# Kernel tuning notes

Measured on AMD Instinct MI355X. Metric: run time of the kernel, lower is better.

The kernel has to match this reference:

```python
import jax, jax.numpy as jnp
import numpy as np

B, N, DH = 8, 2048, 512
EPS = 1e-5


def _layer_norm(x, g, b):
    m = x.mean(-1, keepdims=True)
    v = ((x - m) ** 2).mean(-1, keepdims=True)
    return (x - m) * jax.lax.rsqrt(v + EPS) * g + b


def setup_inputs() -> dict:
    key = jax.random.key(0)
    ks = jax.random.split(key, 20)
    s = 1.0 / np.sqrt(DH)
    sf = 1.0 / np.sqrt(2 * DH)
    return {
        "H": jax.random.normal(ks[0], (B, N, DH), jnp.float32),
        "adj": jax.random.uniform(ks[1], (B, N, N), jnp.float32),
        "hop_emb": jax.random.normal(ks[2], (N, DH), jnp.float32),
        "Wq": jax.random.normal(ks[3], (DH, DH), jnp.float32) * s,
        "bq": jnp.zeros((DH,), jnp.float32),
        "Wk": jax.random.normal(ks[4], (DH, DH), jnp.float32) * s,
        "bk": jnp.zeros((DH,), jnp.float32),
        "Wv": jax.random.normal(ks[5], (DH, DH), jnp.float32) * s,
        "bv": jnp.zeros((DH,), jnp.float32),
        "W1": jax.random.normal(ks[6], (DH, 2 * DH), jnp.float32) * s,
        "b1": jnp.zeros((2 * DH,), jnp.float32),
        "W2": jax.random.normal(ks[7], (2 * DH, DH), jnp.float32) * sf,
        "b2": jnp.zeros((DH,), jnp.float32),
        "g1": jnp.ones((DH,), jnp.float32),
        "be1": jnp.zeros((DH,), jnp.float32),
        "g2": jnp.ones((DH,), jnp.float32),
        "be2": jnp.zeros((DH,), jnp.float32),
    }


def reference(H, adj, hop_emb, Wq, bq, Wk, bk, Wv, bv, W1, b1, W2, b2, g1, be1, g2, be2):
    Q = H @ Wq + bq                                     # [B,N,DH]
    K = H @ Wk + bk
    V = H @ Wv + bv
    scores = jnp.einsum("bid,bjd->bij", Q, K) / np.sqrt(DH).astype(np.float32)
    # (adj[...,None] * hop_emb).mean(-1) == adj * hop_emb.mean(-1)[j]
    hop_effect = adj * hop_emb.mean(-1)[None, None, :]  # [B,N,N]
    attn = jax.nn.softmax(scores * hop_effect, axis=-1)
    attn_out = jnp.einsum("bij,bjd->bid", attn, V)
    x = _layer_norm(attn_out + H, g1, be1)
    ffn = jax.nn.relu(x @ W1 + b1) @ W2 + b2
    return _layer_norm(ffn + x, g2, be2)
```

## Files before the change

kernel.cpp:

```cpp
#include <hip/hip_runtime.h>

typedef unsigned short u16;
typedef __bf16 bf16x8 __attribute__((ext_vector_type(8)));
typedef float f32x4 __attribute__((ext_vector_type(4)));

#define SEQN 2048
#define DHID 512

static __device__ __forceinline__ float bf2f(u16 u) {
    union { unsigned int i; float f; } c; c.i = ((unsigned int)u) << 16; return c.f;
}
static __device__ __forceinline__ u16 f2bf(float f) {
    union { float f; unsigned int i; } c; c.f = f;
    unsigned int x = c.i;
    return (u16)((x + 0x7fffu + ((x >> 16) & 1u)) >> 16);
}

static __device__ __forceinline__ void gld_lds16(const u16* g, u16* l) {
    __builtin_amdgcn_global_load_lds(
        (__attribute__((address_space(1))) void*)(g),
        (__attribute__((address_space(3))) void*)(l), 16, 0, 0);
}

__global__ __launch_bounds__(256) void cvt_kernel(const float* __restrict__ src,
                                                  u16* __restrict__ dst, int n) {
    int i = (blockIdx.x * 256 + threadIdx.x) * 8;
    if (i >= n) return;
    float4 a = *(const float4*)(src + i);
    float4 b = *(const float4*)(src + i + 4);
    union { uint4 u; u16 s[8]; } o;
    o.s[0] = f2bf(a.x); o.s[1] = f2bf(a.y); o.s[2] = f2bf(a.z); o.s[3] = f2bf(a.w);
    o.s[4] = f2bf(b.x); o.s[5] = f2bf(b.y); o.s[6] = f2bf(b.z); o.s[7] = f2bf(b.w);
    *(uint4*)(dst + i) = o.u;
}

__global__ __launch_bounds__(256) void cvt_t_kernel(const float* __restrict__ src,
                                                    u16* __restrict__ dst, int K, int N) {
    int idx = blockIdx.x * 256 + threadIdx.x;
    if (idx >= K * N) return;
    int n = idx / K, k = idx - n * K;
    dst[idx] = f2bf(src[(size_t)k * N + n]);
}

__global__ void hmean_kernel(const float* __restrict__ hop, float* __restrict__ hm) {
    int j = blockIdx.x, t = threadIdx.x;
    const float* p = hop + (size_t)j * DHID + t * 8;
    float4 a = *(const float4*)p;
    float4 b = *(const float4*)(p + 4);
    float s = a.x + a.y + a.z + a.w + b.x + b.y + b.z + b.w;
#pragma unroll
    for (int m = 1; m < 64; m <<= 1) s += __shfl_xor(s, m);
    if (t == 0) hm[j] = s * (1.0f / (float)DHID);
}

enum { EPI_BIAS = 0, EPI_RELU = 1, EPI_SCORES = 2, EPI_PLAIN = 3, EPI_BIAS_T = 4 };

template <int EPI>
__global__ __launch_bounds__(256) void gemm_bt(
    const u16* __restrict__ A, const u16* __restrict__ Bt, u16* __restrict__ C,
    const float* __restrict__ bias, const float* __restrict__ adj,
    const float* __restrict__ hmean,
    int K, int lda, int ldb, int ldc,
    long sA, long sB, long sC, long sAdj, float scale)
{
    __shared__ u16 As[128 * 32];
    __shared__ u16 Bs[128 * 32];

    const int tid = threadIdx.x;
    const int bz = blockIdx.z;
    const u16* Ab = A + (size_t)bz * sA;
    const u16* Bb = Bt + (size_t)bz * sB;
    u16* Cb = C + (size_t)bz * sC;

    const int bm0 = blockIdx.y * 128, bn0 = blockIdx.x * 128;
    const int wid = tid >> 6, lane = tid & 63, quad = lane >> 4, l16 = lane & 15;
    const int wm = (wid >> 1) * 64, wn = (wid & 1) * 64;
    const int srow = lane >> 2;
    const int skof = (lane & 3) * 8;

    f32x4 acc[4][4];
#pragma unroll
    for (int i = 0; i < 4; ++i)
#pragma unroll
        for (int j = 0; j < 4; ++j) acc[i][j] = (f32x4){0.f, 0.f, 0.f, 0.f};

    for (int k0 = 0; k0 < K; k0 += 32) {
#pragma unroll
        for (int it = 0; it < 2; ++it) {
            int c = wid * 2 + it;
            gld_lds16(Ab + (size_t)(bm0 + c * 16 + srow) * lda + k0 + skof,
                      &As[c * 512]);
        }
#pragma unroll
        for (int it = 0; it < 2; ++it) {
            int c = wid * 2 + it;
            gld_lds16(Bb + (size_t)(bn0 + c * 16 + srow) * ldb + k0 + skof,
                      &Bs[c * 512]);
        }
        __syncthreads();

        bf16x8 af[4], bfr[4];
#pragma unroll
        for (int i = 0; i < 4; ++i)
            af[i] = *(const bf16x8*)&As[(wm + i * 16 + l16) * 32 + quad * 8];
#pragma unroll
        for (int j = 0; j < 4; ++j)
            bfr[j] = *(const bf16x8*)&Bs[(wn + j * 16 + l16) * 32 + quad * 8];
#pragma unroll
        for (int i = 0; i < 4; ++i)
#pragma unroll
            for (int j = 0; j < 4; ++j)
                acc[i][j] = __builtin_amdgcn_mfma_f32_16x16x32_bf16(af[i], bfr[j], acc[i][j], 0, 0, 0);
        __syncthreads();
    }

#pragma unroll
    for (int i = 0; i < 4; ++i) {
#pragma unroll
        for (int j = 0; j < 4; ++j) {
            const int gn = bn0 + wn + j * 16 + l16;
            const int gm0 = bm0 + wm + i * 16 + quad * 4;
            if constexpr (EPI == EPI_BIAS || EPI == EPI_RELU) {
                const float b = bias[gn];
#pragma unroll
                for (int r = 0; r < 4; ++r) {
                    float v = acc[i][j][r] + b;
                    if constexpr (EPI == EPI_RELU) v = fmaxf(v, 0.f);
                    Cb[(size_t)(gm0 + r) * ldc + gn] = f2bf(v);
                }
            } else if constexpr (EPI == EPI_SCORES) {
                const float* adjb = adj + (size_t)bz * sAdj;
                const float hmn = hmean[gn];
#pragma unroll
                for (int r = 0; r < 4; ++r) {
                    float v = acc[i][j][r] * scale * adjb[(size_t)(gm0 + r) * ldc + gn] * hmn;
                    Cb[(size_t)(gm0 + r) * ldc + gn] = f2bf(v);
                }
            } else if constexpr (EPI == EPI_BIAS_T) {
                const float b = bias[gn];
                const int bb = gm0 >> 11, n = gm0 & 2047;
                ushort4 o;
                o.x = f2bf(acc[i][j][0] + b);
                o.y = f2bf(acc[i][j][1] + b);
                o.z = f2bf(acc[i][j][2] + b);
                o.w = f2bf(acc[i][j][3] + b);
                *(ushort4*)&C[((size_t)bb * 512 + gn) * 2048 + n] = o;
            } else {
#pragma unroll
                for (int r = 0; r < 4; ++r)
                    Cb[(size_t)(gm0 + r) * ldc + gn] = f2bf(acc[i][j][r]);
            }
        }
    }
}

__global__ __launch_bounds__(256) void softmax_kernel(u16* __restrict__ S) {
    size_t row = blockIdx.x;
    u16* p = S + row * (size_t)SEQN;
    int t = threadIdx.x, wid = t >> 6, lane = t & 63;

    union { uint4 u; u16 s[8]; } d;
    d.u = *(const uint4*)(p + t * 8);
    float v[8];
    float mx = -1e30f;
#pragma unroll
    for (int i = 0; i < 8; ++i) { v[i] = bf2f(d.s[i]); mx = fmaxf(mx, v[i]); }
#pragma unroll
    for (int m = 1; m < 64; m <<= 1) mx = fmaxf(mx, __shfl_xor(mx, m));
    __shared__ float redm[4], reds[4];
    if (lane == 0) redm[wid] = mx;
    __syncthreads();
    mx = fmaxf(fmaxf(redm[0], redm[1]), fmaxf(redm[2], redm[3]));

    float s = 0.f;
#pragma unroll
    for (int i = 0; i < 8; ++i) { v[i] = __expf(v[i] - mx); s += v[i]; }
#pragma unroll
    for (int m = 1; m < 64; m <<= 1) s += __shfl_xor(s, m);
    if (lane == 0) reds[wid] = s;
    __syncthreads();
    s = reds[0] + reds[1] + reds[2] + reds[3];
    float inv = 1.f / s;
#pragma unroll
    for (int i = 0; i < 8; ++i) d.s[i] = f2bf(v[i] * inv);
    *(uint4*)(p + t * 8) = d.u;
}

template <bool B_F32, bool OUT_F32>
__global__ __launch_bounds__(256) void ln_kernel(
    const u16* __restrict__ a, const void* __restrict__ bp,
    const float* __restrict__ g, const float* __restrict__ be,
    void* __restrict__ out)
{
    size_t row = blockIdx.x;
    int t = threadIdx.x, wid = t >> 6, lane = t & 63;
    const u16* pa = a + row * (size_t)DHID;

    unsigned int va = *(const unsigned int*)(pa + t * 2);
    float b0, b1;
    if constexpr (B_F32) {
        float2 vb = *(const float2*)((const float*)bp + row * (size_t)DHID + t * 2);
        b0 = vb.x; b1 = vb.y;
    } else {
        unsigned int vb = *(const unsigned int*)((const u16*)bp + row * (size_t)DHID + t * 2);
        b0 = bf2f((u16)(vb & 0xffff)); b1 = bf2f((u16)(vb >> 16));
    }
    float x0 = bf2f((u16)(va & 0xffff)) + b0;
    float x1 = bf2f((u16)(va >> 16)) + b1;
    float s = x0 + x1, sq = x0 * x0 + x1 * x1;
#pragma unroll
    for (int m = 1; m < 64; m <<= 1) { s += __shfl_xor(s, m); sq += __shfl_xor(sq, m); }
    __shared__ float rs[4], rq[4];
    if (lane == 0) { rs[wid] = s; rq[wid] = sq; }
    __syncthreads();
    s = rs[0] + rs[1] + rs[2] + rs[3];
    sq = rq[0] + rq[1] + rq[2] + rq[3];
    float mean = s * (1.f / (float)DHID);
    float var = sq * (1.f / (float)DHID) - mean * mean;
    float rstd = rsqrtf(var + 1e-5f);

    float2 vg = *(const float2*)(g + t * 2);
    float2 vbe = *(const float2*)(be + t * 2);
    float y0 = (x0 - mean) * rstd * vg.x + vbe.x;
    float y1 = (x1 - mean) * rstd * vg.y + vbe.y;
    if constexpr (OUT_F32) {
        *(float2*)((float*)out + row * (size_t)DHID + t * 2) = make_float2(y0, y1);
    } else {
        unsigned int o = (unsigned int)f2bf(y0) | ((unsigned int)f2bf(y1) << 16);
        *(unsigned int*)((u16*)out + row * (size_t)DHID + t * 2) = o;
    }
}

extern "C" void kernel_launch(void* const* d_in, const int* in_sizes, int n_in,
                              void* d_out, int out_size, void* d_ws, size_t ws_size,
                              hipStream_t stream) {
    const float* H   = (const float*)d_in[0];
    const float* adj = (const float*)d_in[1];
    const float* hop = (const float*)d_in[2];
    const float* Wq  = (const float*)d_in[3];
    const float* bq  = (const float*)d_in[4];
    const float* Wk  = (const float*)d_in[5];
    const float* bk  = (const float*)d_in[6];
    const float* Wv  = (const float*)d_in[7];
    const float* bv  = (const float*)d_in[8];
    const float* W1  = (const float*)d_in[9];
    const float* b1  = (const float*)d_in[10];
    const float* W2  = (const float*)d_in[11];
    const float* b2  = (const float*)d_in[12];
    const float* g1  = (const float*)d_in[13];
    const float* be1 = (const float*)d_in[14];
    const float* g2  = (const float*)d_in[15];
    const float* be2 = (const float*)d_in[16];

    const size_t MiB = 1ull << 20;
    char* w = (char*)d_ws;
    float* hm  = (float*)w;
    u16* Hb   = (u16*)(w + 1 * MiB);
    u16* Wqt  = (u16*)(w + 17 * MiB);
    u16* Wkt  = (u16*)(w + 17 * MiB + 512 * 1024);
    u16* Wvt  = (u16*)(w + 18 * MiB);
    u16* W1t  = (u16*)(w + 18 * MiB + 512 * 1024);
    u16* W2t  = (u16*)(w + 19 * MiB + 512 * 1024);
    u16* Q    = (u16*)(w + 21 * MiB);
    u16* Kb   = (u16*)(w + 37 * MiB);
    u16* Vt   = (u16*)(w + 53 * MiB);
    u16* S    = (u16*)(w + 69 * MiB);
    u16* AO  = Q;
    u16* X   = Kb;
    u16* F2  = Vt;
    u16* HID = S;

    const int BN = 8, N = SEQN, D = DHID;
    const long nd = (long)N * D, nn = (long)N * N;
    const float scale = 0.044194173824159216f;

    const int groups = (ws_size >= 133 * MiB) ? 1 : 2;
    const int gb = BN / groups;

    cvt_kernel<<<(BN * N * D) / (8 * 256), 256, 0, stream>>>(H, Hb, BN * N * D);
    cvt_t_kernel<<<(D * D + 255) / 256, 256, 0, stream>>>(Wq, Wqt, D, D);
    cvt_t_kernel<<<(D * D + 255) / 256, 256, 0, stream>>>(Wk, Wkt, D, D);
    cvt_t_kernel<<<(D * D + 255) / 256, 256, 0, stream>>>(Wv, Wvt, D, D);
    cvt_t_kernel<<<(D * 2 * D + 255) / 256, 256, 0, stream>>>(W1, W1t, D, 2 * D);
    cvt_t_kernel<<<(2 * D * D + 255) / 256, 256, 0, stream>>>(W2, W2t, 2 * D, D);

    hmean_kernel<<<N, 64, 0, stream>>>(hop, hm);

    gemm_bt<EPI_BIAS><<<dim3(4, 128, 1), 256, 0, stream>>>(
        Hb, Wqt, Q, bq, nullptr, nullptr, D, D, D, D, 0, 0, 0, 0, 0.f);
    gemm_bt<EPI_BIAS><<<dim3(4, 128, 1), 256, 0, stream>>>(
        Hb, Wkt, Kb, bk, nullptr, nullptr, D, D, D, D, 0, 0, 0, 0, 0.f);
    gemm_bt<EPI_BIAS_T><<<dim3(4, 128, 1), 256, 0, stream>>>(
        Hb, Wvt, Vt, bv, nullptr, nullptr, D, D, D, D, 0, 0, 0, 0, 0.f);

    for (int g = 0; g < groups; ++g) {
        const u16* Qg = Q + (size_t)g * gb * nd;
        const u16* Kg = Kb + (size_t)g * gb * nd;
        const u16* Vg = Vt + (size_t)g * gb * nd;
        const float* adjg = adj + (size_t)g * gb * nn;
        u16* AOg = AO + (size_t)g * gb * nd;

        gemm_bt<EPI_SCORES><<<dim3(16, 16, gb), 256, 0, stream>>>(
            Qg, Kg, S, nullptr, adjg, hm, D, D, D, N, nd, nd, nn, nn, scale);

        softmax_kernel<<<gb * N, 256, 0, stream>>>(S);

        gemm_bt<EPI_PLAIN><<<dim3(4, 16, gb), 256, 0, stream>>>(
            S, Vg, AOg, nullptr, nullptr, nullptr, N, N, N, D, nn, nd, nd, 0, 0.f);
    }

    ln_kernel<true, false><<<BN * N, 256, 0, stream>>>(AO, H, g1, be1, X);

    gemm_bt<EPI_RELU><<<dim3(8, 128, 1), 256, 0, stream>>>(
        X, W1t, HID, b1, nullptr, nullptr, D, D, D, 2 * D, 0, 0, 0, 0, 0.f);

    gemm_bt<EPI_BIAS><<<dim3(4, 128, 1), 256, 0, stream>>>(
        HID, W2t, F2, b2, nullptr, nullptr, 2 * D, 2 * D, 2 * D, D, 0, 0, 0, 0, 0.f);

    ln_kernel<false, true><<<BN * N, 256, 0, stream>>>(F2, X, g2, be2, (float*)d_out);
}
```

Baseline: 589.6 us.

## Fuse scores, softmax and PV into a single flash-style attention kernel

Result: no change. 595.9 us (+1.1%).

```diff
diff --git a/kernel.cpp b/kernel.cpp
--- a/kernel.cpp
+++ b/kernel.cpp
@@ -53,15 +53,14 @@
     if (t == 0) hm[j] = s * (1.0f / (float)DHID);
 }
 
-enum { EPI_BIAS = 0, EPI_RELU = 1, EPI_SCORES = 2, EPI_PLAIN = 3, EPI_BIAS_T = 4 };
+enum { EPI_BIAS = 0, EPI_RELU = 1, EPI_PLAIN = 3, EPI_BIAS_T = 4 };
 
 template <int EPI>
 __global__ __launch_bounds__(256) void gemm_bt(
     const u16* __restrict__ A, const u16* __restrict__ Bt, u16* __restrict__ C,
-    const float* __restrict__ bias, const float* __restrict__ adj,
-    const float* __restrict__ hmean,
+    const float* __restrict__ bias,
     int K, int lda, int ldb, int ldc,
-    long sA, long sB, long sC, long sAdj, float scale)
+    long sA, long sB, long sC)
 {
     __shared__ u16 As[128 * 32];
     __shared__ u16 Bs[128 * 32];
@@ -126,14 +125,6 @@
                 for (int r = 0; r < 4; ++r) {
                     float v = acc[i][j][r] + b;
                     if constexpr (EPI == EPI_RELU) v = fmaxf(v, 0.f);
-                    Cb[(size_t)(gm0 + r) * ldc + gn] = f2bf(v);
-                }
-            } else if constexpr (EPI == EPI_SCORES) {
-                const float* adjb = adj + (size_t)bz * sAdj;
-                const float hmn = hmean[gn];
-#pragma unroll
-                for (int r = 0; r < 4; ++r) {
-                    float v = acc[i][j][r] * scale * adjb[(size_t)(gm0 + r) * ldc + gn] * hmn;
                     Cb[(size_t)(gm0 + r) * ldc + gn] = f2bf(v);
                 }
             } else if constexpr (EPI == EPI_BIAS_T) {
@@ -154,36 +145,118 @@
     }
 }
 
-__global__ __launch_bounds__(256) void softmax_kernel(u16* __restrict__ S) {
-    size_t row = blockIdx.x;
-    u16* p = S + row * (size_t)SEQN;
-    int t = threadIdx.x, wid = t >> 6, lane = t & 63;
-
-    union { uint4 u; u16 s[8]; } d;
-    d.u = *(const uint4*)(p + t * 8);
-    float v[8];
-    float mx = -1e30f;
-#pragma unroll
-    for (int i = 0; i < 8; ++i) { v[i] = bf2f(d.s[i]); mx = fmaxf(mx, v[i]); }
-#pragma unroll
-    for (int m = 1; m < 64; m <<= 1) mx = fmaxf(mx, __shfl_xor(mx, m));
-    __shared__ float redm[4], reds[4];
-    if (lane == 0) redm[wid] = mx;
-    __syncthreads();
-    mx = fmaxf(fmaxf(redm[0], redm[1]), fmaxf(redm[2], redm[3]));
-
-    float s = 0.f;
-#pragma unroll
-    for (int i = 0; i < 8; ++i) { v[i] = __expf(v[i] - mx); s += v[i]; }
-#pragma unroll
-    for (int m = 1; m < 64; m <<= 1) s += __shfl_xor(s, m);
-    if (lane == 0) reds[wid] = s;
-    __syncthreads();
-    s = reds[0] + reds[1] + reds[2] + reds[3];
-    float inv = 1.f / s;
-#pragma unroll
-    for (int i = 0; i < 8; ++i) d.s[i] = f2bf(v[i] * inv);
-    *(uint4*)(p + t * 8) = d.u;
+__global__ __launch_bounds__(256, 1) void attn_kernel(
+    const u16* __restrict__ Q, const u16* __restrict__ K, const u16* __restrict__ Vt,
+    const float* __restrict__ adj, const float* __restrict__ hm,
+    u16* __restrict__ AO)
+{
+    extern __shared__ u16 lds[];
+    u16* Ks = lds;
+    u16* Vs = lds + 16384;
+
+    const int tid = threadIdx.x, wid = tid >> 6, lane = tid & 63;
+    const int quad = lane >> 4, l16 = lane & 15;
+    const int b = blockIdx.x;
+    const int q0w = blockIdx.y * 64 + wid * 16;
+    const int srow = lane >> 2, sko = (lane & 3) * 8;
+
+    const u16* Qg = Q + (size_t)b * SEQN * DHID;
+    const u16* Kg = K + (size_t)b * SEQN * DHID;
+    const u16* Vg = Vt + (size_t)b * DHID * SEQN;
+    const float* adjg = adj + (size_t)b * SEQN * SEQN;
+    u16* AOg = AO + (size_t)b * SEQN * DHID;
+    u16* Plds = lds + wid * 640;
+
+    const float scale = 0.044194173824159216f;
+
+    bf16x8 qf[16];
+#pragma unroll
+    for (int ds = 0; ds < 16; ++ds)
+        qf[ds] = *(const bf16x8*)(Qg + (size_t)(q0w + l16) * DHID + ds * 32 + quad * 8);
+
+    f32x4 oacc[32];
+#pragma unroll
+    for (int dt = 0; dt < 32; ++dt) oacc[dt] = (f32x4){0.f, 0.f, 0.f, 0.f};
+    float lsum[4] = {0.f, 0.f, 0.f, 0.f};
+
+    for (int kt = 0; kt < 64; ++kt) {
+        const int kv0 = kt * 32;
+
+#pragma unroll
+        for (int i = 0; i < 8; ++i) {
+            int id = wid * 8 + i;
+            int ds = id >> 1, c = id & 1;
+            gld_lds16(Kg + (size_t)(kv0 + c * 16 + srow) * DHID + ds * 32 + sko,
+                      &Ks[ds * 1024 + c * 512]);
+        }
+        __syncthreads();
+
+#pragma unroll
+        for (int i = 0; i < 8; ++i) {
+            int id = wid * 8 + i;
+            gld_lds16(Vg + (size_t)(id * 16 + srow) * SEQN + kv0 + sko,
+                      &Vs[id * 512]);
+        }
+
+        float hv0 = hm[kv0 + l16] * scale;
+        float hv1 = hm[kv0 + 16 + l16] * scale;
+        float av[8];
+        const float* arow = adjg + (size_t)(q0w + quad * 4) * SEQN + kv0;
+#pragma unroll
+        for (int r = 0; r < 4; ++r) {
+            av[r]     = arow[(size_t)r * SEQN + l16];
+            av[4 + r] = arow[(size_t)r * SEQN + 16 + l16];
+        }
+
+        f32x4 s0a = {0.f,0.f,0.f,0.f}, s0b = {0.f,0.f,0.f,0.f};
+        f32x4 s1a = {0.f,0.f,0.f,0.f}, s1b = {0.f,0.f,0.f,0.f};
+#pragma unroll
+        for (int ds = 0; ds < 16; ds += 2) {
+            bf16x8 k00 = *(const bf16x8*)&Ks[ds * 1024 + l16 * 32 + quad * 8];
+            bf16x8 k01 = *(const bf16x8*)&Ks[ds * 1024 + 512 + l16 * 32 + quad * 8];
+            s0a = __builtin_amdgcn_mfma_f32_16x16x32_bf16(qf[ds], k00, s0a, 0, 0, 0);
+            s1a = __builtin_amdgcn_mfma_f32_16x16x32_bf16(qf[ds], k01, s1a, 0, 0, 0);
+            bf16x8 k10 = *(const bf16x8*)&Ks[(ds + 1) * 1024 + l16 * 32 + quad * 8];
+            bf16x8 k11 = *(const bf16x8*)&Ks[(ds + 1) * 1024 + 512 + l16 * 32 + quad * 8];
+            s0b = __builtin_amdgcn_mfma_f32_16x16x32_bf16(qf[ds + 1], k10, s0b, 0, 0, 0);
+            s1b = __builtin_amdgcn_mfma_f32_16x16x32_bf16(qf[ds + 1], k11, s1b, 0, 0, 0);
+        }
+        f32x4 s0 = s0a + s0b, s1 = s1a + s1b;
+        __syncthreads();
+
+#pragma unroll
+        for (int r = 0; r < 4; ++r) {
+            float p0 = __expf(s0[r] * av[r] * hv0);
+            float p1 = __expf(s1[r] * av[4 + r] * hv1);
+            lsum[r] += p0 + p1;
+            Plds[(quad * 4 + r) * 40 + l16] = f2bf(p0);
+            Plds[(quad * 4 + r) * 40 + 16 + l16] = f2bf(p1);
+        }
+        asm volatile("s_waitcnt lgkmcnt(0)" ::: "memory");
+
+        bf16x8 pf = *(const bf16x8*)&Plds[l16 * 40 + quad * 8];
+#pragma unroll
+        for (int dt = 0; dt < 32; ++dt) {
+            bf16x8 vf = *(const bf16x8*)&Vs[(dt * 16 + l16) * 32 + quad * 8];
+            oacc[dt] = __builtin_amdgcn_mfma_f32_16x16x32_bf16(pf, vf, oacc[dt], 0, 0, 0);
+        }
+        __syncthreads();
+    }
+
+#pragma unroll
+    for (int r = 0; r < 4; ++r) {
+#pragma unroll
+        for (int m = 1; m < 16; m <<= 1) lsum[r] += __shfl_xor(lsum[r], m);
+        lsum[r] = 1.f / lsum[r];
+    }
+#pragma unroll
+    for (int dt = 0; dt < 32; ++dt) {
+#pragma unroll
+        for (int r = 0; r < 4; ++r) {
+            AOg[(size_t)(q0w + quad * 4 + r) * DHID + dt * 16 + l16] =
+                f2bf(oacc[dt][r] * lsum[r]);
+        }
+    }
 }
 
 template <bool B_F32, bool OUT_F32>
@@ -264,18 +337,13 @@
     u16* Q    = (u16*)(w + 21 * MiB);
     u16* Kb   = (u16*)(w + 37 * MiB);
     u16* Vt   = (u16*)(w + 53 * MiB);
-    u16* S    = (u16*)(w + 69 * MiB);
-    u16* AO  = Q;
+    u16* AO   = (u16*)(w + 69 * MiB);
+    u16* HID  = (u16*)(w + 85 * MiB);
     u16* X   = Kb;
     u16* F2  = Vt;
-    u16* HID = S;
 
     const int BN = 8, N = SEQN, D = DHID;
-    const long nd = (long)N * D, nn = (long)N * N;
-    const float scale = 0.044194173824159216f;
-
-    const int groups = (ws_size >= 133 * MiB) ? 1 : 2;
-    const int gb = BN / groups;
+    const long nd = (long)N * D;
 
     cvt_kernel<<<(BN * N * D) / (8 * 256), 256, 0, stream>>>(H, Hb, BN * N * D);
     cvt_t_kernel<<<(D * D + 255) / 256, 256, 0, stream>>>(Wq, Wqt, D, D);
@@ -287,35 +355,21 @@
     hmean_kernel<<<N, 64, 0, stream>>>(hop, hm);
 
     gemm_bt<EPI_BIAS><<<dim3(4, 128, 1), 256, 0, stream>>>(
-        Hb, Wqt, Q, bq, nullptr, nullptr, D, D, D, D, 0, 0, 0, 0, 0.f);
+        Hb, Wqt, Q, bq, D, D, D, D, 0, 0, 0);
     gemm_bt<EPI_BIAS><<<dim3(4, 128, 1), 256, 0, stream>>>(
-        Hb, Wkt, Kb, bk, nullptr, nullptr, D, D, D, D, 0, 0, 0, 0, 0.f);
+        Hb, Wkt, Kb, bk, D, D, D, D, 0, 0, 0);
     gemm_bt<EPI_BIAS_T><<<dim3(4, 128, 1), 256, 0, stream>>>(
-        Hb, Wvt, Vt, bv, nullptr, nullptr, D, D, D, D, 0, 0, 0, 0, 0.f);
-
-    for (int g = 0; g < groups; ++g) {
-        const u16* Qg = Q + (size_t)g * gb * nd;
-        const u16* Kg = Kb + (size_t)g * gb * nd;
-        const u16* Vg = Vt + (size_t)g * gb * nd;
-        const float* adjg = adj + (size_t)g * gb * nn;
-        u16* AOg = AO + (size_t)g * gb * nd;
-
-        gemm_bt<EPI_SCORES><<<dim3(16, 16, gb), 256, 0, stream>>>(
-            Qg, Kg, S, nullptr, adjg, hm, D, D, D, N, nd, nd, nn, nn, scale);
-
-        softmax_kernel<<<gb * N, 256, 0, stream>>>(S);
-
-        gemm_bt<EPI_PLAIN><<<dim3(4, 16, gb), 256, 0, stream>>>(
-            S, Vg, AOg, nullptr, nullptr, nullptr, N, N, N, D, nn, nd, nd, 0, 0.f);
-    }
+        Hb, Wvt, Vt, bv, D, D, D, D, 0, 0, 0);
+
+    attn_kernel<<<dim3(8, 32), 256, 65536, stream>>>(Q, Kb, Vt, adj, hm, AO);
 
     ln_kernel<true, false><<<BN * N, 256, 0, stream>>>(AO, H, g1, be1, X);
 
     gemm_bt<EPI_RELU><<<dim3(8, 128, 1), 256, 0, stream>>>(
-        X, W1t, HID, b1, nullptr, nullptr, D, D, D, 2 * D, 0, 0, 0, 0, 0.f);
+        X, W1t, HID, b1, D, D, D, 2 * D, 0, 0, 0);
 
     gemm_bt<EPI_BIAS><<<dim3(4, 128, 1), 256, 0, stream>>>(
-        HID, W2t, F2, b2, nullptr, nullptr, 2 * D, 2 * D, 2 * D, D, 0, 0, 0, 0, 0.f);
+        HID, W2t, F2, b2, 2 * D, 2 * D, 2 * D, D, 0, 0, 0);
 
     ln_kernel<false, true><<<BN * N, 256, 0, stream>>>(F2, X, g2, be2, (float*)d_out);
 }
```
